# Optimization experiments

Measured on AMD Instinct MI355X. Metric: run time of the kernel, lower is better.

Reference implementation:

```python
import jax, jax.numpy as jnp
import numpy as np

B, C_IN, C_OUT, H, F_DIM = 32, 64, 1, 4096, 8
OUT_CH, K = F_DIM + 1, F_DIM // 2 + 1          # even-feature branch: 9 channels, kernel (1,5)
HALF = F_DIM * (F_DIM + 1) // 2                # 36 upper-triangular entries
MIN_VEC = 0.001
IU = np.triu_indices(F_DIM)                    # torch.triu_indices(f, f)


def setup_inputs() -> dict:
    key = jax.random.key(0)
    k1, k2, k3, k4, k5 = jax.random.split(key, 5)
    x = jax.random.normal(k1, (B, C_IN, H, F_DIM), jnp.float32)
    w_n = jax.random.normal(k2, (C_OUT, C_IN, 1, 1), jnp.float32) * 0.05
    b_n = jax.random.normal(k3, (C_OUT,), jnp.float32) * 0.05
    w_p = jax.random.normal(k4, (OUT_CH, C_IN, 1, K), jnp.float32) * 0.05
    b_p = jax.random.normal(k5, (OUT_CH,), jnp.float32) * 0.05
    return {"x": x, "w_n": w_n, "b_n": b_n, "w_p": w_p, "b_p": b_p}


def _forward(x, w_n, b_n, w_p, b_p):
    # n_conv: 1x1 conv -> softplus  (loc: [B, C_OUT, H, F_DIM])
    loc = jax.nn.softplus(
        jnp.einsum('bchw,oc->bohw', x, w_n[:, :, 0, 0]) + b_n[None, :, None, None])
    # p_conv: (1,K) valid conv -> softplus  (scale: [B, OUT_CH, H, W_out])
    p = jax.lax.conv_general_dilated(
        x, w_p, window_strides=(1, 1), padding='VALID',
        dimension_numbers=('NCHW', 'OIHW', 'NCHW')) + b_p[None, :, None, None]
    scale = jax.nn.softplus(p)
    # unsqueeze(1) + permute(0,1,3,2,4) + flatten(start_dim=3) -> [B,1,H,HALF]
    sigma = jnp.transpose(scale, (0, 2, 1, 3)).reshape(B, 1, H, HALF)
    # scatter upper-tri values symmetrically into [B,1,H,F,F]
    z = jnp.zeros((B, 1, H, F_DIM, F_DIM), sigma.dtype)
    z = z.at[..., IU[0], IU[1]].set(sigma)
    z = z.at[..., IU[1], IU[0]].set(sigma)
    # batched eigh, clamp eigenvalues, reconstruct PD matrix, symmetrize
    eigval, eigvec = jnp.linalg.eigh(z)
    clamped = jnp.maximum(eigval, MIN_VEC)
    pd = jnp.einsum('...ij,...j,...kj->...ik', eigvec, clamped, eigvec)
    pd = 0.5 * (pd + jnp.swapaxes(pd, -1, -2))
    return loc, pd


def reference(x, w_n, b_n, w_p, b_p):
    return _forward(x, w_n, b_n, w_p, b_p)
```

## Files before the change

kernel.cpp:

```cpp
#include <hip/hip_runtime.h>
#include <math.h>

#define B_      32
#define C_IN    64
#define H_      4096
#define F_      8
#define OUT_CH  9
#define KW      5
#define BH      (B_ * H_)
#define LOC_N   (BH * F_)
#define NSWEEP  6
#define MIN_VEC 0.001f

__device__ __forceinline__ float softplus_f(float v) {
    return fmaxf(v, 0.0f) + __logf(1.0f + __expf(-fabsf(v)));
}

__global__ __launch_bounds__(256, 2)
void mgauss_fused(const float* __restrict__ x,
                  const float* __restrict__ w_n,
                  const float* __restrict__ b_n,
                  const float* __restrict__ w_p,
                  const float* __restrict__ b_p,
                  float* __restrict__ out)
{
    const int t = blockIdx.x * 256 + threadIdx.x;
    const int b = t >> 12;
    const int h = t & 4095;

    const float* xp = x + ((size_t)b * C_IN * H_ + h) * F_;

    float la[F_];
    #pragma unroll
    for (int w = 0; w < F_; ++w) la[w] = 0.0f;
    float pa[OUT_CH][4];
    #pragma unroll
    for (int o = 0; o < OUT_CH; ++o)
        #pragma unroll
        for (int wo = 0; wo < 4; ++wo) pa[o][wo] = 0.0f;

    #pragma unroll 2
    for (int c = 0; c < C_IN; ++c) {
        const float4 x0 = *(const float4*)(xp + (size_t)c * (H_ * F_));
        const float4 x1 = *(const float4*)(xp + (size_t)c * (H_ * F_) + 4);
        const float xa[F_] = {x0.x, x0.y, x0.z, x0.w, x1.x, x1.y, x1.z, x1.w};

        const float wn = w_n[c];
        #pragma unroll
        for (int w = 0; w < F_; ++w) la[w] = fmaf(xa[w], wn, la[w]);

        #pragma unroll
        for (int o = 0; o < OUT_CH; ++o) {
            #pragma unroll
            for (int k = 0; k < KW; ++k) {
                const float wv = w_p[(o * C_IN + c) * KW + k];
                #pragma unroll
                for (int wo = 0; wo < 4; ++wo)
                    pa[o][wo] = fmaf(xa[wo + k], wv, pa[o][wo]);
            }
        }
    }

    {
        const float bn = b_n[0];
        float lv[F_];
        #pragma unroll
        for (int w = 0; w < F_; ++w) lv[w] = softplus_f(la[w] + bn);
        float* lo = out + (size_t)t * F_;
        *(float4*)(lo)     = make_float4(lv[0], lv[1], lv[2], lv[3]);
        *(float4*)(lo + 4) = make_float4(lv[4], lv[5], lv[6], lv[7]);
    }

    float sig[36];
    #pragma unroll
    for (int o = 0; o < OUT_CH; ++o) {
        const float bp = b_p[o];
        #pragma unroll
        for (int wo = 0; wo < 4; ++wo)
            sig[o * 4 + wo] = softplus_f(pa[o][wo] + bp);
    }

    float A[F_][F_];
    {
        int k = 0;
        #pragma unroll
        for (int i = 0; i < F_; ++i)
            #pragma unroll
            for (int j = i; j < F_; ++j) {
                A[i][j] = sig[k];
                A[j][i] = sig[k];
                ++k;
            }
    }

    float V[F_][F_];
    #pragma unroll
    for (int i = 0; i < F_; ++i)
        #pragma unroll
        for (int j = 0; j < F_; ++j)
            V[i][j] = (i == j) ? 1.0f : 0.0f;

    for (int sweep = 0; sweep < NSWEEP; ++sweep) {
        #pragma unroll
        for (int p = 0; p < F_ - 1; ++p) {
            #pragma unroll
            for (int q = p + 1; q < F_; ++q) {
                const float apq = A[p][q];
                const float app = A[p][p];
                const float aqq = A[q][q];
                float th = (aqq - app) / (2.0f * apq);
                float tt = 1.0f / (fabsf(th) + sqrtf(fmaf(th, th, 1.0f)));
                tt = (th < 0.0f) ? -tt : tt;
                tt = (apq == 0.0f) ? 0.0f : tt;
                const float cc = 1.0f / sqrtf(fmaf(tt, tt, 1.0f));
                const float ss = tt * cc;

                #pragma unroll
                for (int i = 0; i < F_; ++i) {
                    const float u = A[p][i], v = A[q][i];
                    A[p][i] = cc * u - ss * v;
                    A[q][i] = fmaf(ss, u, cc * v);
                }
                #pragma unroll
                for (int i = 0; i < F_; ++i) {
                    const float u = A[i][p], v = A[i][q];
                    A[i][p] = cc * u - ss * v;
                    A[i][q] = fmaf(ss, u, cc * v);
                }
                #pragma unroll
                for (int i = 0; i < F_; ++i) {
                    const float u = V[i][p], v = V[i][q];
                    V[i][p] = cc * u - ss * v;
                    V[i][q] = fmaf(ss, u, cc * v);
                }
            }
        }
    }

    float lam[F_];
    #pragma unroll
    for (int k = 0; k < F_; ++k) lam[k] = fmaxf(A[k][k], MIN_VEC);

    float W[F_][F_];
    #pragma unroll
    for (int i = 0; i < F_; ++i)
        #pragma unroll
        for (int k = 0; k < F_; ++k)
            W[i][k] = V[i][k] * lam[k];

    float PD[F_][F_];
    #pragma unroll
    for (int i = 0; i < F_; ++i) {
        #pragma unroll
        for (int j = i; j < F_; ++j) {
            float acc = 0.0f;
            #pragma unroll
            for (int k = 0; k < F_; ++k)
                acc = fmaf(W[i][k], V[j][k], acc);
            PD[i][j] = acc;
            PD[j][i] = acc;
        }
    }

    float* po = out + LOC_N + (size_t)t * (F_ * F_);
    #pragma unroll
    for (int i = 0; i < F_; ++i) {
        *(float4*)(po + i * F_)     = make_float4(PD[i][0], PD[i][1], PD[i][2], PD[i][3]);
        *(float4*)(po + i * F_ + 4) = make_float4(PD[i][4], PD[i][5], PD[i][6], PD[i][7]);
    }
}

extern "C" void kernel_launch(void* const* d_in, const int* in_sizes, int n_in,
                              void* d_out, int out_size, void* d_ws, size_t ws_size,
                              hipStream_t stream) {
    const float* x   = (const float*)d_in[0];
    const float* w_n = (const float*)d_in[1];
    const float* b_n = (const float*)d_in[2];
    const float* w_p = (const float*)d_in[3];
    const float* b_p = (const float*)d_in[4];
    float* out = (float*)d_out;

    dim3 grid(BH / 256);
    dim3 block(256);
    hipLaunchKernelGGL(mgauss_fused, grid, block, 0, stream,
                       x, w_n, b_n, w_p, b_p, out);
}
```

Measured before the change: 478.4 us.

## Use round-robin parallel Jacobi ordering with upper-triangle-only symmetric rotation updates

Replaces the cyclic-by-row Jacobi sweep with a round-robin order of 7 rounds, each holding 4 disjoint rotations. All 4 rotation angles are computed before they are applied, which exposes independent work to the scheduler. The A update keeps only the upper triangle: diagonal entries are updated in closed form and the pivot is zeroed, so roughly half the A arithmetic goes away. The channel loop unroll also rises from 2 to 4. The risk is that the compiler cannot constant-fold the PAIRS table loads, which would push A into scratch memory; the new ordering may also change accuracy slightly at a fixed sweep count.

```diff
diff --git a/kernel.cpp b/kernel.cpp
--- a/kernel.cpp
+++ b/kernel.cpp
@@ -11,6 +11,18 @@
 #define LOC_N   (BH * F_)
 #define NSWEEP  6
 #define MIN_VEC 0.001f
+
+__device__ const int PAIRS[7][4][2] = {
+  {{0,7},{1,6},{2,5},{3,4}},
+  {{0,6},{5,7},{1,4},{2,3}},
+  {{0,5},{4,6},{3,7},{1,2}},
+  {{0,4},{3,5},{2,6},{1,7}},
+  {{0,3},{2,4},{1,5},{6,7}},
+  {{0,2},{1,3},{4,7},{5,6}},
+  {{0,1},{2,7},{3,6},{4,5}},
+};
+
+#define SYM(i,j) (((i) < (j)) ? A[i][j] : A[j][i])
 
 __device__ __forceinline__ float softplus_f(float v) {
     return fmaxf(v, 0.0f) + __logf(1.0f + __expf(-fabsf(v)));
@@ -39,7 +51,7 @@
         #pragma unroll
         for (int wo = 0; wo < 4; ++wo) pa[o][wo] = 0.0f;
 
-    #pragma unroll 2
+    #pragma unroll 4
     for (int c = 0; c < C_IN; ++c) {
         const float4 x0 = *(const float4*)(xp + (size_t)c * (H_ * F_));
         const float4 x1 = *(const float4*)(xp + (size_t)c * (H_ * F_) + 4);
@@ -71,24 +83,22 @@
         *(float4*)(lo + 4) = make_float4(lv[4], lv[5], lv[6], lv[7]);
     }
 
-    float sig[36];
-    #pragma unroll
-    for (int o = 0; o < OUT_CH; ++o) {
-        const float bp = b_p[o];
-        #pragma unroll
-        for (int wo = 0; wo < 4; ++wo)
-            sig[o * 4 + wo] = softplus_f(pa[o][wo] + bp);
-    }
-
     float A[F_][F_];
     {
+        float sig[36];
+        #pragma unroll
+        for (int o = 0; o < OUT_CH; ++o) {
+            const float bp = b_p[o];
+            #pragma unroll
+            for (int wo = 0; wo < 4; ++wo)
+                sig[o * 4 + wo] = softplus_f(pa[o][wo] + bp);
+        }
         int k = 0;
         #pragma unroll
         for (int i = 0; i < F_; ++i)
             #pragma unroll
             for (int j = i; j < F_; ++j) {
                 A[i][j] = sig[k];
-                A[j][i] = sig[k];
                 ++k;
             }
     }
@@ -102,9 +112,11 @@
 
     for (int sweep = 0; sweep < NSWEEP; ++sweep) {
         #pragma unroll
-        for (int p = 0; p < F_ - 1; ++p) {
-            #pragma unroll
-            for (int q = p + 1; q < F_; ++q) {
+        for (int r = 0; r < 7; ++r) {
+            float cs[4], sn[4], tv[4];
+            #pragma unroll
+            for (int j = 0; j < 4; ++j) {
+                const int p = PAIRS[r][j][0], q = PAIRS[r][j][1];
                 const float apq = A[p][q];
                 const float app = A[p][p];
                 const float aqq = A[q][q];
@@ -113,25 +125,34 @@
                 tt = (th < 0.0f) ? -tt : tt;
                 tt = (apq == 0.0f) ? 0.0f : tt;
                 const float cc = 1.0f / sqrtf(fmaf(tt, tt, 1.0f));
-                const float ss = tt * cc;
-
+                cs[j] = cc; sn[j] = tt * cc; tv[j] = tt;
+            }
+            #pragma unroll
+            for (int j = 0; j < 4; ++j) {
+                const int p = PAIRS[r][j][0], q = PAIRS[r][j][1];
+                const float cc = cs[j], ss = sn[j], tt = tv[j];
+                const float apq = A[p][q];
+                A[p][p] = fmaf(-tt, apq, A[p][p]);
+                A[q][q] = fmaf( tt, apq, A[q][q]);
+                A[p][q] = 0.0f;
                 #pragma unroll
                 for (int i = 0; i < F_; ++i) {
-                    const float u = A[p][i], v = A[q][i];
-                    A[p][i] = cc * u - ss * v;
-                    A[q][i] = fmaf(ss, u, cc * v);
+                    if (i == p || i == q) continue;
+                    const float aip = SYM(i, p);
+                    const float aiq = SYM(i, q);
+                    SYM(i, p) = fmaf(-ss, aiq, cc * aip);
+                    SYM(i, q) = fmaf( ss, aip, cc * aiq);
                 }
-                #pragma unroll
-                for (int i = 0; i < F_; ++i) {
-                    const float u = A[i][p], v = A[i][q];
-                    A[i][p] = cc * u - ss * v;
-                    A[i][q] = fmaf(ss, u, cc * v);
-                }
+            }
+            #pragma unroll
+            for (int j = 0; j < 4; ++j) {
+                const int p = PAIRS[r][j][0], q = PAIRS[r][j][1];
+                const float cc = cs[j], ss = sn[j];
                 #pragma unroll
                 for (int i = 0; i < F_; ++i) {
                     const float u = V[i][p], v = V[i][q];
-                    V[i][p] = cc * u - ss * v;
-                    V[i][q] = fmaf(ss, u, cc * v);
+                    V[i][p] = fmaf(-ss, v, cc * u);
+                    V[i][q] = fmaf( ss, u, cc * v);
                 }
             }
         }
```

After: 458.0 us. 4.3% less time.
